# Kernel optimization log

Measured on AMD Instinct MI355X. Metric: run time of the kernel, lower is better.

Reference implementation:

```python
import jax, jax.numpy as jnp
import numpy as np

N_NODES = 131072
N_EDGES = 1048576
N_GRAPHS = 1024
EMB = 96
HID = 64
OUT = 3
NEG_SLOPE = 0.2  # PyG GATConv default leaky_relu slope


def setup_inputs() -> dict:
    key = jax.random.key(0)
    ks = jax.random.split(key, 8)
    x = jax.random.normal(ks[0], (N_NODES, EMB), dtype=jnp.float32)
    edge_index = jax.random.randint(ks[1], (2, N_EDGES), 0, N_NODES, dtype=jnp.int64)
    batch = jnp.sort(jax.random.randint(ks[2], (N_NODES,), 0, N_GRAPHS, dtype=jnp.int64))
    s = 1.0 / np.sqrt(EMB)
    W = jax.random.uniform(ks[3], (EMB, HID), jnp.float32, -s, s)       # GATConv lin (no bias)
    att_src = jax.random.uniform(ks[4], (HID,), jnp.float32, -s, s)     # a_src
    att_dst = jax.random.uniform(ks[5], (HID,), jnp.float32, -s, s)     # a_dst
    bias_gat = jnp.zeros((HID,), jnp.float32)
    sf = 1.0 / np.sqrt(HID)
    fc_w = jax.random.uniform(ks[6], (OUT, HID), jnp.float32, -sf, sf)
    fc_b = jax.random.uniform(ks[7], (OUT,), jnp.float32, -sf, sf)
    return {"x": x, "edge_index": edge_index, "batch": batch, "W": W,
            "att_src": att_src, "att_dst": att_dst, "bias_gat": bias_gat,
            "fc_w": fc_w, "fc_b": fc_b}


def _segment_softmax(logits, seg, num_segments):
    # numerically stable softmax over edges grouped by target node
    m = jax.ops.segment_max(logits, seg, num_segments=num_segments)
    e = jnp.exp(logits - m[seg])
    z = jax.ops.segment_sum(e, seg, num_segments=num_segments)
    return e / (z[seg] + 1e-16)


def reference(x, edge_index, batch, W, att_src, att_dst, bias_gat, fc_w, fc_b):
    N = x.shape[0]
    # PyG GATConv (heads=1): add self loops
    loop = jnp.arange(N, dtype=edge_index.dtype)
    src = jnp.concatenate([edge_index[0], loop])
    dst = jnp.concatenate([edge_index[1], loop])

    h = x @ W                                    # [N, HID]
    a_s = h @ att_src                            # [N]
    a_d = h @ att_dst                            # [N]
    logits = jax.nn.leaky_relu(a_s[src] + a_d[dst], NEG_SLOPE)  # [E]
    alpha = _segment_softmax(logits, dst, N)     # softmax over in-edges per target
    out = jax.ops.segment_sum(alpha[:, None] * h[src], dst, num_segments=N)
    out = out + bias_gat                         # [N, HID]

    # global_mean_pool over graphs
    sums = jax.ops.segment_sum(out, batch, num_segments=N_GRAPHS)
    cnt = jax.ops.segment_sum(jnp.ones((N,), out.dtype), batch, num_segments=N_GRAPHS)
    pooled = sums / jnp.maximum(cnt, 1.0)[:, None]  # [G, HID]

    logits_out = pooled @ fc_w.T + fc_b          # [G, OUT]
    return jax.nn.log_softmax(logits_out, axis=1)
```

## Files before the change

### kernel.cpp

```cpp
#include <hip/hip_runtime.h>
#include <hip/hip_fp16.h>

#define N_NODES 131072
#define N_EDGES 1048576
#define N_GRAPHS 1024
#define EMB 96
#define HID 64
#define OUT 3
#define CAP 32
#define NBKT 512
#define NCHUNK 512
#define BCAP2 20

typedef _Float16 half8 __attribute__((ext_vector_type(8)));
typedef float float4v __attribute__((ext_vector_type(4)));

__global__ __launch_bounds__(512, 4) void k_front(
    const int* __restrict__ src, const int* __restrict__ dst,
    int* __restrict__ ebuf, int* __restrict__ ccnt,
    const float* __restrict__ x, const float* __restrict__ W,
    const float* __restrict__ att_src, const float* __restrict__ att_dst,
    __half* __restrict__ h, float* __restrict__ a_s, float* __restrict__ a_d,
    float* __restrict__ poolz)
{
    int tid = threadIdx.x;
    __shared__ _Float16 lwt[64 * 104];
    __shared__ int bcnt[NBKT];

    if (blockIdx.x < NCHUNK) {
        int blk = blockIdx.x;
        bcnt[tid] = 0;
        if (blk < 33) {
            int idx = blk * 512 + tid;
            if (idx < (N_GRAPHS * HID + N_GRAPHS) / 4)
                ((float4*)poolz)[idx] = (float4){0.f, 0.f, 0.f, 0.f};
        }
        __syncthreads();
        int e0 = blk * 2048;
        #pragma unroll
        for (int i = 0; i < 4; ++i) {
            int e = e0 + i * 512 + tid;
            int sv = src[e], dv = dst[e];
            int b = dv >> 8;
            int r = atomicAdd(&bcnt[b], 1);
            if (r < BCAP2)
                ebuf[((size_t)b * NCHUNK + blk) * BCAP2 + r] = (sv << 8) | (dv & 255);
        }
        __syncthreads();
        int v = bcnt[tid];
        ccnt[tid * NCHUNK + blk] = v < BCAP2 ? v : BCAP2;
    } else {
        int sub = blockIdx.x - NCHUNK;
        #pragma unroll
        for (int i = 0; i < 12; ++i) {
            int idx = i * 512 + tid;
            lwt[(idx & 63) * 104 + (idx >> 6)] = (_Float16)W[idx];
        }
        __syncthreads();

        int lane = tid & 63;
        int w = tid >> 6;
        int m16 = lane & 15;
        int quad = lane >> 4;
        int rowbase = sub * 128 + w * 16;

        half8 bf[4][3];
        #pragma unroll
        for (int nt = 0; nt < 4; ++nt)
            #pragma unroll
            for (int kb = 0; kb < 3; ++kb)
                bf[nt][kb] = *(const half8*)(lwt + (nt * 16 + m16) * 104
                                             + kb * 32 + quad * 8);

        float4v acc[4];
        #pragma unroll
        for (int nt = 0; nt < 4; ++nt)
            acc[nt] = (float4v){0.f, 0.f, 0.f, 0.f};

        const float* xrow = x + (size_t)(rowbase + m16) * EMB + quad * 8;
        #pragma unroll
        for (int kb = 0; kb < 3; ++kb) {
            float4 xa = *(const float4*)(xrow + kb * 32);
            float4 xb = *(const float4*)(xrow + kb * 32 + 4);
            half8 af;
            af[0] = (_Float16)xa.x; af[1] = (_Float16)xa.y;
            af[2] = (_Float16)xa.z; af[3] = (_Float16)xa.w;
            af[4] = (_Float16)xb.x; af[5] = (_Float16)xb.y;
            af[6] = (_Float16)xb.z; af[7] = (_Float16)xb.w;
            #pragma unroll
            for (int nt = 0; nt < 4; ++nt)
                acc[nt] = __builtin_amdgcn_mfma_f32_16x16x32_f16(
                    af, bf[nt][kb], acc[nt], 0, 0, 0);
        }

        float asv[4], adv[4];
        #pragma unroll
        for (int nt = 0; nt < 4; ++nt) {
            asv[nt] = att_src[nt * 16 + m16];
            adv[nt] = att_dst[nt * 16 + m16];
        }

        #pragma unroll
        for (int r = 0; r < 4; ++r) {
            int row = rowbase + quad * 4 + r;
            float ps = 0.f, pd = 0.f;
            #pragma unroll
            for (int nt = 0; nt < 4; ++nt) {
                float v = acc[nt][r];
                h[(size_t)row * HID + nt * 16 + m16] = __float2half(v);
                ps += v * asv[nt];
                pd += v * adv[nt];
            }
            #pragma unroll
            for (int off = 8; off >= 1; off >>= 1) {
                ps += __shfl_xor(ps, off, 64);
                pd += __shfl_xor(pd, off, 64);
            }
            if (m16 == 0) { a_s[row] = ps; a_d[row] = pd; }
        }
    }
}

__global__ __launch_bounds__(512) void k_place(const int* __restrict__ ebuf,
    const int* __restrict__ ccnt, int* __restrict__ cnt, int* __restrict__ slots)
{
    int tid = threadIdx.x;
    int b = blockIdx.x;
    __shared__ int lists[256 * CAP];
    __shared__ int cl[256];
    __shared__ int cm[NCHUNK];
    if (tid < 256) cl[tid] = 0;
    cm[tid] = ccnt[b * NCHUNK + tid];
    __syncthreads();
    const int* eb = ebuf + (size_t)b * NCHUNK * BCAP2;
    #pragma unroll 1
    for (int it0 = 0; it0 < 20; it0 += 5) {
        int e[5];
        #pragma unroll
        for (int k = 0; k < 5; ++k)
            e[k] = eb[(it0 + k) * 512 + tid];
        #pragma unroll
        for (int k = 0; k < 5; ++k) {
            int off = (it0 + k) * 512 + tid;
            int c = off / BCAP2, s = off % BCAP2;
            if (s < cm[c]) {
                int local = e[k] & 255;
                int slot = atomicAdd(&cl[local], 1);
                if (slot < CAP)
                    lists[local * CAP + slot] = e[k] >> 8;
            }
        }
    }
    __syncthreads();
    int* sb = slots + (size_t)b * 256 * CAP;
    #pragma unroll
    for (int it = 0; it < 16; ++it)
        sb[it * 512 + tid] = lists[it * 512 + tid];
    if (tid < 256) {
        int v = cl[tid];
        cnt[b * 256 + tid] = v < CAP ? v : CAP;
    }
}

__global__ __launch_bounds__(256, 6) void k_accum(const __half2* __restrict__ h2,
    const float* __restrict__ a_s, const float* __restrict__ a_d,
    const int* __restrict__ cnt, const int* __restrict__ slots,
    const float* __restrict__ bias, __half2* __restrict__ out)
{
    int tid = threadIdx.x;
    int lane = tid & 63;
    int sub = lane & 31;
    int gbase = lane & 32;
    int node = blockIdx.x * 8 + ((tid >> 6) << 1) + (gbase >> 5);

    int deg = cnt[node];
    int sv = slots[(size_t)node * CAP + sub];
    if (deg > CAP) deg = CAP;
    int s_j = (sub < deg) ? sv : node;

    __half2 hv = h2[(size_t)node * 32 + sub];
    __half2 hg[16];
    #pragma unroll
    for (int k = 0; k < 16; ++k) {
        int i = __shfl(s_j, gbase + k, 64);
        hg[k] = h2[(size_t)i * 32 + sub];
    }
    float asg = a_s[s_j];
    float adi = a_d[node];
    float asi = a_s[node];

    float t = asg + adi;
    t = t > 0.f ? t : 0.2f * t;
    float w_j = (sub < deg) ? __expf(t) : 0.f;

    float t0 = asi + adi;
    t0 = t0 > 0.f ? t0 : 0.2f * t0;
    float w0 = __expf(t0);

    float z = w_j;
    #pragma unroll
    for (int off = 16; off >= 1; off >>= 1) z += __shfl_xor(z, off, 64);
    z += w0;

    float2 acc;
    acc.x = w0 * __half2float(hv.x);
    acc.y = w0 * __half2float(hv.y);
    #pragma unroll
    for (int k = 0; k < 16; ++k) {
        float wk = __shfl(w_j, gbase + k, 64);
        acc.x += wk * __half2float(hg[k].x);
        acc.y += wk * __half2float(hg[k].y);
    }

    for (int j0 = 16; j0 < deg; j0 += 8) {
        __half2 g2[8];
        #pragma unroll
        for (int k = 0; k < 8; ++k) {
            int i = __shfl(s_j, gbase + j0 + k, 64);
            g2[k] = h2[(size_t)i * 32 + sub];
        }
        #pragma unroll
        for (int k = 0; k < 8; ++k) {
            float wk = __shfl(w_j, gbase + j0 + k, 64);
            acc.x += wk * __half2float(g2[k].x);
            acc.y += wk * __half2float(g2[k].y);
        }
    }

    float inv = 1.f / (z + 1e-16f);
    float2 b2 = ((const float2*)bias)[sub];
    out[(size_t)node * 32 + sub] =
        __floats2half2_rn(acc.x * inv + b2.x, acc.y * inv + b2.y);
}

__global__ __launch_bounds__(256) void k_pool(const __half* __restrict__ out,
    const int* __restrict__ batch, float* __restrict__ pool,
    float* __restrict__ gcnt)
{
    int lane = threadIdx.x & 63;
    int wv = blockIdx.x * 4 + (threadIdx.x >> 6);
    int base = wv * 64;
    int bv = batch[base + lane];
    int g_cur = __shfl(bv, 0);
    float acc = 0.f;
    int run = 0;
    for (int c = 0; c < 8; ++c) {
        int n0 = base + c * 8;
        float v[8];
        #pragma unroll
        for (int k = 0; k < 8; ++k)
            v[k] = __half2float(out[(size_t)(n0 + k) * HID + lane]);
        int b0 = __shfl(bv, c * 8);
        int b7 = __shfl(bv, c * 8 + 7);
        if (b0 == b7) {
            if (b0 != g_cur) {
                atomicAdd(&pool[g_cur * HID + lane], acc);
                if (lane == 0) atomicAdd(&gcnt[g_cur], (float)run);
                acc = 0.f; run = 0; g_cur = b0;
            }
            acc += ((v[0] + v[1]) + (v[2] + v[3]))
                 + ((v[4] + v[5]) + (v[6] + v[7]));
            run += 8;
        } else {
            #pragma unroll
            for (int k = 0; k < 8; ++k) {
                int g = __shfl(bv, c * 8 + k);
                if (g != g_cur) {
                    atomicAdd(&pool[g_cur * HID + lane], acc);
                    if (lane == 0) atomicAdd(&gcnt[g_cur], (float)run);
                    acc = 0.f; run = 0; g_cur = g;
                }
                acc += v[k]; ++run;
            }
        }
    }
    atomicAdd(&pool[g_cur * HID + lane], acc);
    if (lane == 0) atomicAdd(&gcnt[g_cur], (float)run);
}

__global__ __launch_bounds__(256) void k_head(const float* __restrict__ pool,
    const float* __restrict__ gcnt, const float* __restrict__ fc_w,
    const float* __restrict__ fc_b, float* __restrict__ out)
{
    int tid = threadIdx.x;
    int lane = tid & 63;
    int g = blockIdx.x * 4 + (tid >> 6);
    float p = pool[g * HID + lane] / fmaxf(gcnt[g], 1.0f);
    float l0 = p * fc_w[0 * HID + lane];
    float l1 = p * fc_w[1 * HID + lane];
    float l2 = p * fc_w[2 * HID + lane];
    #pragma unroll
    for (int off = 32; off >= 1; off >>= 1) {
        l0 += __shfl_xor(l0, off, 64);
        l1 += __shfl_xor(l1, off, 64);
        l2 += __shfl_xor(l2, off, 64);
    }
    l0 += fc_b[0]; l1 += fc_b[1]; l2 += fc_b[2];
    float m = fmaxf(l0, fmaxf(l1, l2));
    float lse = m + logf(__expf(l0 - m) + __expf(l1 - m) + __expf(l2 - m));
    if (lane == 0) {
        out[g * 3 + 0] = l0 - lse;
        out[g * 3 + 1] = l1 - lse;
        out[g * 3 + 2] = l2 - lse;
    }
}

extern "C" void kernel_launch(void* const* d_in, const int* in_sizes, int n_in,
                              void* d_out, int out_size, void* d_ws, size_t ws_size,
                              hipStream_t stream)
{
    const float* x        = (const float*)d_in[0];
    const int*   ei       = (const int*)d_in[1];
    const int*   batch    = (const int*)d_in[2];
    const float* W        = (const float*)d_in[3];
    const float* att_src  = (const float*)d_in[4];
    const float* att_dst  = (const float*)d_in[5];
    const float* bias_gat = (const float*)d_in[6];
    const float* fc_w     = (const float*)d_in[7];
    const float* fc_b     = (const float*)d_in[8];
    float* out = (float*)d_out;

    char* ws = (char*)d_ws;
    size_t off = 0;
    auto alloc = [&](size_t bytes) {
        void* p = ws + off;
        off += (bytes + 255) & ~(size_t)255;
        return p;
    };
    __half* h    = (__half*)alloc((size_t)N_NODES * HID * 2);
    int*   slots = (int*)  alloc((size_t)N_NODES * CAP * 4);
    int*   cnt   = (int*)  alloc((size_t)N_NODES * 4);
    float* pool  = (float*)alloc((size_t)N_GRAPHS * HID * 4);
    float* gcnt  = (float*)alloc((size_t)N_GRAPHS * 4);
    float* a_s   = (float*)alloc((size_t)N_NODES * 4);
    float* a_d   = (float*)alloc((size_t)N_NODES * 4);
    int*   ccnt  = (int*)  alloc((size_t)NBKT * NCHUNK * 4);
    int*   ebuf  = (int*)alloc((size_t)NBKT * NCHUNK * BCAP2 * 4);
    __half* nout = (__half*)ebuf;

    const int* e_src = ei;
    const int* e_dst = ei + N_EDGES;

    k_front<<<NCHUNK + 1024, 512, 0, stream>>>(e_src, e_dst, ebuf, ccnt,
                                               x, W, att_src, att_dst,
                                               h, a_s, a_d, pool);
    k_place<<<NBKT, 512, 0, stream>>>(ebuf, ccnt, cnt, slots);
    k_accum<<<N_NODES / 8, 256, 0, stream>>>((const __half2*)h, a_s, a_d, cnt,
                                             slots, bias_gat, (__half2*)nout);
    k_pool <<<N_NODES / 256, 256, 0, stream>>>(nout, batch, pool, gcnt);
    k_head <<<N_GRAPHS / 4, 256, 0, stream>>>(pool, gcnt, fc_w, fc_b, out);
}
```

Before: 164.8 us.

## Fuse edge placement with attention accumulation and restage edge buckets through LDS

Merges the bucket-placement kernel into the attention aggregation kernel, so each of 512 blocks builds its per-node adjacency lists in shared memory and then aggregates its 256 nodes directly. This removes the global slots/cnt round trip and one launch. The front kernel now stages the first 16 edges per bucket in LDS and writes chunk-major 32-wide padded segments, giving coalesced writes. The trade-off is that aggregation runs on only 512 blocks at 2 blocks per SM with a sequential 16-pass loop, which lowers parallelism and latency hiding for the gathers. The per-chunk bucket capacity rises from 20 to 32.

Result: faster. 161.1 us (-2.3%).

```diff
diff --git a/kernel.cpp b/kernel.cpp
--- a/kernel.cpp
+++ b/kernel.cpp
@@ -10,7 +10,8 @@
 #define CAP 32
 #define NBKT 512
 #define NCHUNK 512
-#define BCAP2 20
+#define BCAP 32
+#define LCAP 16
 
 typedef _Float16 half8 __attribute__((ext_vector_type(8)));
 typedef float float4v __attribute__((ext_vector_type(4)));
@@ -24,11 +25,12 @@
     float* __restrict__ poolz)
 {
     int tid = threadIdx.x;
-    __shared__ _Float16 lwt[64 * 104];
-    __shared__ int bcnt[NBKT];
+    __shared__ int smem[NBKT * LCAP + NBKT];
 
     if (blockIdx.x < NCHUNK) {
         int blk = blockIdx.x;
+        int* lists16 = smem;
+        int* bcnt = smem + NBKT * LCAP;
         bcnt[tid] = 0;
         if (blk < 33) {
             int idx = blk * 512 + tid;
@@ -42,15 +44,25 @@
             int e = e0 + i * 512 + tid;
             int sv = src[e], dv = dst[e];
             int b = dv >> 8;
+            int packed = (sv << 8) | (dv & 255);
             int r = atomicAdd(&bcnt[b], 1);
-            if (r < BCAP2)
-                ebuf[((size_t)b * NCHUNK + blk) * BCAP2 + r] = (sv << 8) | (dv & 255);
+            if (r < LCAP)
+                lists16[b * LCAP + r] = packed;
+            else if (r < BCAP)
+                ebuf[((size_t)blk * NBKT + b) * BCAP + r] = packed;
         }
         __syncthreads();
+        #pragma unroll
+        for (int it = 0; it < 16; ++it) {
+            int idx = it * 512 + tid;
+            int seg = idx >> 4, s = idx & 15;
+            ebuf[((size_t)blk * NBKT + seg) * BCAP + s] = lists16[idx];
+        }
         int v = bcnt[tid];
-        ccnt[tid * NCHUNK + blk] = v < BCAP2 ? v : BCAP2;
+        ccnt[blk * NBKT + tid] = v < BCAP ? v : BCAP;
     } else {
         int sub = blockIdx.x - NCHUNK;
+        _Float16* lwt = (_Float16*)smem;
         #pragma unroll
         for (int i = 0; i < 12; ++i) {
             int idx = i * 512 + tid;
@@ -121,8 +133,11 @@
     }
 }
 
-__global__ __launch_bounds__(512) void k_place(const int* __restrict__ ebuf,
-    const int* __restrict__ ccnt, int* __restrict__ cnt, int* __restrict__ slots)
+__global__ __launch_bounds__(512, 2) void k_place_accum(
+    const int* __restrict__ ebuf, const int* __restrict__ ccnt,
+    const __half2* __restrict__ h2, const float* __restrict__ a_s,
+    const float* __restrict__ a_d, const float* __restrict__ bias,
+    __half2* __restrict__ out)
 {
     int tid = threadIdx.x;
     int b = blockIdx.x;
@@ -130,20 +145,21 @@
     __shared__ int cl[256];
     __shared__ int cm[NCHUNK];
     if (tid < 256) cl[tid] = 0;
-    cm[tid] = ccnt[b * NCHUNK + tid];
+    cm[tid] = ccnt[tid * NBKT + b];
     __syncthreads();
-    const int* eb = ebuf + (size_t)b * NCHUNK * BCAP2;
+
     #pragma unroll 1
-    for (int it0 = 0; it0 < 20; it0 += 5) {
-        int e[5];
-        #pragma unroll
-        for (int k = 0; k < 5; ++k)
-            e[k] = eb[(it0 + k) * 512 + tid];
-        #pragma unroll
-        for (int k = 0; k < 5; ++k) {
-            int off = (it0 + k) * 512 + tid;
-            int c = off / BCAP2, s = off % BCAP2;
-            if (s < cm[c]) {
+    for (int it0 = 0; it0 < 32; it0 += 4) {
+        int e[4];
+        #pragma unroll
+        for (int k = 0; k < 4; ++k) {
+            int c = (it0 + k) * 16 + (tid >> 5);
+            e[k] = ebuf[((size_t)c * NBKT + b) * BCAP + (tid & 31)];
+        }
+        #pragma unroll
+        for (int k = 0; k < 4; ++k) {
+            int c = (it0 + k) * 16 + (tid >> 5);
+            if ((tid & 31) < cm[c]) {
                 int local = e[k] & 255;
                 int slot = atomicAdd(&cl[local], 1);
                 if (slot < CAP)
@@ -152,85 +168,73 @@
         }
     }
     __syncthreads();
-    int* sb = slots + (size_t)b * 256 * CAP;
-    #pragma unroll
-    for (int it = 0; it < 16; ++it)
-        sb[it * 512 + tid] = lists[it * 512 + tid];
-    if (tid < 256) {
-        int v = cl[tid];
-        cnt[b * 256 + tid] = v < CAP ? v : CAP;
-    }
-}
-
-__global__ __launch_bounds__(256, 6) void k_accum(const __half2* __restrict__ h2,
-    const float* __restrict__ a_s, const float* __restrict__ a_d,
-    const int* __restrict__ cnt, const int* __restrict__ slots,
-    const float* __restrict__ bias, __half2* __restrict__ out)
-{
-    int tid = threadIdx.x;
+
     int lane = tid & 63;
     int sub = lane & 31;
     int gbase = lane & 32;
-    int node = blockIdx.x * 8 + ((tid >> 6) << 1) + (gbase >> 5);
-
-    int deg = cnt[node];
-    int sv = slots[(size_t)node * CAP + sub];
-    if (deg > CAP) deg = CAP;
-    int s_j = (sub < deg) ? sv : node;
-
-    __half2 hv = h2[(size_t)node * 32 + sub];
-    __half2 hg[16];
-    #pragma unroll
-    for (int k = 0; k < 16; ++k) {
-        int i = __shfl(s_j, gbase + k, 64);
-        hg[k] = h2[(size_t)i * 32 + sub];
-    }
-    float asg = a_s[s_j];
-    float adi = a_d[node];
-    float asi = a_s[node];
-
-    float t = asg + adi;
-    t = t > 0.f ? t : 0.2f * t;
-    float w_j = (sub < deg) ? __expf(t) : 0.f;
-
-    float t0 = asi + adi;
-    t0 = t0 > 0.f ? t0 : 0.2f * t0;
-    float w0 = __expf(t0);
-
-    float z = w_j;
-    #pragma unroll
-    for (int off = 16; off >= 1; off >>= 1) z += __shfl_xor(z, off, 64);
-    z += w0;
-
-    float2 acc;
-    acc.x = w0 * __half2float(hv.x);
-    acc.y = w0 * __half2float(hv.y);
-    #pragma unroll
-    for (int k = 0; k < 16; ++k) {
-        float wk = __shfl(w_j, gbase + k, 64);
-        acc.x += wk * __half2float(hg[k].x);
-        acc.y += wk * __half2float(hg[k].y);
-    }
-
-    for (int j0 = 16; j0 < deg; j0 += 8) {
-        __half2 g2[8];
-        #pragma unroll
-        for (int k = 0; k < 8; ++k) {
-            int i = __shfl(s_j, gbase + j0 + k, 64);
-            g2[k] = h2[(size_t)i * 32 + sub];
-        }
-        #pragma unroll
-        for (int k = 0; k < 8; ++k) {
-            float wk = __shfl(w_j, gbase + j0 + k, 64);
-            acc.x += wk * __half2float(g2[k].x);
-            acc.y += wk * __half2float(g2[k].y);
-        }
-    }
-
-    float inv = 1.f / (z + 1e-16f);
+    int wv = tid >> 6;
     float2 b2 = ((const float2*)bias)[sub];
-    out[(size_t)node * 32 + sub] =
-        __floats2half2_rn(acc.x * inv + b2.x, acc.y * inv + b2.y);
+
+    for (int p = 0; p < 16; ++p) {
+        int local = p * 16 + wv * 2 + (gbase >> 5);
+        int node = b * 256 + local;
+        int deg = cl[local]; if (deg > CAP) deg = CAP;
+        int sv = lists[local * CAP + sub];
+        int s_j = (sub < deg) ? sv : node;
+
+        __half2 hv = h2[(size_t)node * 32 + sub];
+        __half2 hg[16];
+        #pragma unroll
+        for (int k = 0; k < 16; ++k) {
+            int i = __shfl(s_j, gbase + k, 64);
+            hg[k] = h2[(size_t)i * 32 + sub];
+        }
+        float asg = a_s[s_j];
+        float adi = a_d[node];
+        float asi = a_s[node];
+
+        float t = asg + adi;
+        t = t > 0.f ? t : 0.2f * t;
+        float w_j = (sub < deg) ? __expf(t) : 0.f;
+
+        float t0 = asi + adi;
+        t0 = t0 > 0.f ? t0 : 0.2f * t0;
+        float w0 = __expf(t0);
+
+        float z = w_j;
+        #pragma unroll
+        for (int off = 16; off >= 1; off >>= 1) z += __shfl_xor(z, off, 64);
+        z += w0;
+
+        float2 acc;
+        acc.x = w0 * __half2float(hv.x);
+        acc.y = w0 * __half2float(hv.y);
+        #pragma unroll
+        for (int k = 0; k < 16; ++k) {
+            float wk = __shfl(w_j, gbase + k, 64);
+            acc.x += wk * __half2float(hg[k].x);
+            acc.y += wk * __half2float(hg[k].y);
+        }
+
+        for (int j0 = 16; j0 < deg; j0 += 8) {
+            __half2 g2[8];
+            #pragma unroll
+            for (int k = 0; k < 8; ++k) {
+                int i = __shfl(s_j, gbase + j0 + k, 64);
+                g2[k] = h2[(size_t)i * 32 + sub];
+            }
+            #pragma unroll
+            for (int k = 0; k < 8; ++k) {
+                float wk = __shfl(w_j, gbase + j0 + k, 64);
+                acc.x += wk * __half2float(g2[k].x);
+                acc.y += wk * __half2float(g2[k].y);
+            }
+        }
+
+        float inv = 1.f / (z + 1e-16f);
+        out[(size_t)node * 32 + sub] =
+            __floats2half2_rn(acc.x * inv + b2.x, acc.y * inv + b2.y);
+    }
 }
 
 __global__ __launch_bounds__(256) void k_pool(const __half* __restrict__ out,
@@ -328,15 +332,13 @@
         return p;
     };
     __half* h    = (__half*)alloc((size_t)N_NODES * HID * 2);
-    int*   slots = (int*)  alloc((size_t)N_NODES * CAP * 4);
-    int*   cnt   = (int*)  alloc((size_t)N_NODES * 4);
     float* pool  = (float*)alloc((size_t)N_GRAPHS * HID * 4);
     float* gcnt  = (float*)alloc((size_t)N_GRAPHS * 4);
     float* a_s   = (float*)alloc((size_t)N_NODES * 4);
     float* a_d   = (float*)alloc((size_t)N_NODES * 4);
-    int*   ccnt  = (int*)  alloc((size_t)NBKT * NCHUNK * 4);
-    int*   ebuf  = (int*)alloc((size_t)NBKT * NCHUNK * BCAP2 * 4);
-    __half* nout = (__half*)ebuf;
+    int*   ccnt  = (int*)  alloc((size_t)NCHUNK * NBKT * 4);
+    int*   ebuf  = (int*)  alloc((size_t)NCHUNK * NBKT * BCAP * 4);
+    __half* nout = (__half*)alloc((size_t)N_NODES * HID * 2);
 
     const int* e_src = ei;
     const int* e_dst = ei + N_EDGES;
@@ -344,9 +346,8 @@
     k_front<<<NCHUNK + 1024, 512, 0, stream>>>(e_src, e_dst, ebuf, ccnt,
                                                x, W, att_src, att_dst,
                                                h, a_s, a_d, pool);
-    k_place<<<NBKT, 512, 0, stream>>>(ebuf, ccnt, cnt, slots);
-    k_accum<<<N_NODES / 8, 256, 0, stream>>>((const __half2*)h, a_s, a_d, cnt,
-                                             slots, bias_gat, (__half2*)nout);
+    k_place_accum<<<NBKT, 512, 0, stream>>>(ebuf, ccnt, (const __half2*)h,
+                                            a_s, a_d, bias_gat, (__half2*)nout);
     k_pool <<<N_NODES / 256, 256, 0, stream>>>(nout, batch, pool, gcnt);
     k_head <<<N_GRAPHS / 4, 256, 0, stream>>>(pool, gcnt, fc_w, fc_b, out);
 }
```
